# Kernel optimization log

Measured on AMD Instinct MI355X. Metric: run time of the kernel, lower is better.

The kernel has to match this reference:

```python
import jax, jax.numpy as jnp
import numpy as np

V, N, K, D = 2, 100000, 8, 128
TAU = 1.0
LOG_2PI = float(np.log(2.0 * np.pi))


def setup_inputs() -> dict:
    key = jax.random.key(0)
    k1, k2, k3 = jax.random.split(key, 3)
    z = jax.random.normal(k1, (V, N, D), dtype=jnp.float32)
    phi = jnp.ones((V, K), dtype=jnp.float32) / K
    mu = jax.random.normal(k2, (V, K, D), dtype=jnp.float32)
    # sigma: identity (as in torch init) plus a small symmetric PSD perturbation
    a = 0.05 * jax.random.normal(k3, (V, K, D, D), dtype=jnp.float32)
    sigma = jnp.eye(D, dtype=jnp.float32) + jnp.einsum('vkde,vkfe->vkdf', a, a)
    return {"z": z, "phi": phi, "mu": mu, "sigma": sigma}


def _compute_energy(z, phi, mu, sigma):
    # z: [N, D]; phi: [K]; mu: [K, D]; sigma: [K, D, D]
    eps_eye = 1e-6 * jnp.eye(D, dtype=z.dtype)
    sigma_stable = sigma + eps_eye  # [K, D, D]
    inv_sigma = jnp.linalg.inv(sigma_stable)
    det_sigma = jnp.clip(jnp.linalg.det(sigma_stable), 1e-6, None)  # [K]
    diff = z[:, None, :] - mu[None, :, :]  # [N, K, D]
    maha = jnp.einsum('nkd,kde,nke->nk', diff, inv_sigma, diff)  # [N, K]
    log_pi = jax.nn.log_softmax(phi)  # [K]
    log_prob = (-0.5 * maha
                - 0.5 * D * LOG_2PI
                - 0.5 * jnp.log(det_sigma)[None, :]
                + log_pi[None, :])  # [N, K]
    energy = -jax.nn.logsumexp(log_prob, axis=1)  # [N]
    penalty = jnp.sum(1.0 / (jnp.diagonal(sigma_stable, axis1=-2, axis2=-1) + 1e-12))
    return energy, penalty


def reference(z, phi, mu, sigma):
    # vmap over views; energies_v: [V, N]
    energies_v, penalties = jax.vmap(_compute_energy)(z, phi, mu, sigma)
    energies = energies_v.T  # [N, V]
    total_energies = jnp.sum(energies)
    total_penalty = jnp.sum(penalties)
    weights = jax.nn.softmax(-energies / TAU, axis=1)  # [N, V]
    return energies, weights, total_energies, total_penalty
```

## Files before the change

### kernel.cpp

```cpp
#include <hip/hip_runtime.h>
#include <math.h>

#define V 2
#define NN 100000
#define KK 8
#define DD 128
#define TILE_N 128
#define SL 132
#define NT 782
#define CH 8
#define CPX 13
#define NPAD 100096
#define LOG2PI 1.8378770664093454f
#define LOG_1EM6 -13.815510557964274f

#define IMG_PB 40960
#define IMG_LO_US 10240

#define LF_B   1114112
#define LF_STRIDE 69632
#define BV_B   2228224
#define C_B    2236416
#define MAHA_B 2236480

#define OUT_W_OFF (NN*V)
#define OUT_TE (2*NN*V)
#define OUT_TP (2*NN*V + 1)

typedef __attribute__((ext_vector_type(8))) short bf16x8;
typedef __attribute__((ext_vector_type(4))) float f32x4;
typedef __attribute__((ext_vector_type(4))) unsigned u32x4;

__device__ __forceinline__ unsigned short f2bf_rtn(float f) {
    unsigned u = __builtin_bit_cast(unsigned, f);
    unsigned r = u + 0x7FFFu + ((u >> 16) & 1u);
    return (unsigned short)(r >> 16);
}
__device__ __forceinline__ float bf2f(unsigned short h) {
    unsigned u = ((unsigned)h) << 16;
    return __builtin_bit_cast(float, u);
}

__device__ __forceinline__ void cvt_pair(float f0, float f1, unsigned& hi, unsigned& lo) {
    unsigned u0 = __builtin_bit_cast(unsigned, f0);
    unsigned u1 = __builtin_bit_cast(unsigned, f1);
    hi = __builtin_amdgcn_perm(u1, u0, 0x07060302u);
    float r0 = f0 - __builtin_bit_cast(float, u0 & 0xFFFF0000u);
    float r1 = f1 - __builtin_bit_cast(float, u1 & 0xFFFF0000u);
    unsigned v0 = __builtin_bit_cast(unsigned, r0) + 0x8000u;
    unsigned v1 = __builtin_bit_cast(unsigned, r1) + 0x8000u;
    lo = __builtin_amdgcn_perm(v1, v0, 0x07060302u);
}

__global__ void zero_kernel(float* out) {
    int t = threadIdx.x;
    if (t < 2) out[OUT_TE + t] = 0.0f;
}

__global__ __launch_bounds__(256) void prep_chol(const float* __restrict__ phi,
                                                 const float* __restrict__ mu,
                                                 const float* __restrict__ sigma,
                                                 void* __restrict__ wsv,
                                                 float* __restrict__ out) {
    __shared__ float Lf[DD * SL];
    __shared__ float P[8][SL];
    __shared__ float dvec[DD];
    __shared__ float mulds[DD];
    __shared__ float red[256];
    __shared__ float Bv[8];
    __shared__ float Bb[DD];

    const int tid = threadIdx.x;
    const int vk  = blockIdx.x;
    const int v   = vk >> 3;
    const int k   = vk & 7;
    const int R   = tid >> 4;
    const int C   = tid & 15;

    if (tid < DD) mulds[tid] = mu[vk * DD + tid];

    float A[8][8];
    const float* sig = sigma + (size_t)vk * DD * DD;
    float pen = 0.0f;
    #pragma unroll
    for (int a = 0; a < 8; ++a) {
        const float4* p4 = (const float4*)(sig + (size_t)(8 * R + a) * DD + 8 * C);
        float4 x = p4[0], y = p4[1];
        A[a][0] = x.x; A[a][1] = x.y; A[a][2] = x.z; A[a][3] = x.w;
        A[a][4] = y.x; A[a][5] = y.y; A[a][6] = y.z; A[a][7] = y.w;
        if (R == C) A[a][a] += 1e-6f;
    }
    if (R == C) {
        #pragma unroll
        for (int a = 0; a < 8; ++a) pen += 1.0f / (A[a][a] + 1e-12f);
    }

    for (int i = tid; i < DD * SL; i += 256) Lf[i] = 0.0f;

    red[tid] = pen;
    __syncthreads();
    for (int s = 128; s > 0; s >>= 1) {
        if (tid < s) red[tid] += red[tid + s];
        __syncthreads();
    }
    if (tid == 0) atomicAdd(&out[OUT_TP], red[0]);
    __syncthreads();

    for (int p = 0; p < 16; ++p) {
        if (C == p && R >= p) {
            #pragma unroll
            for (int b = 0; b < 8; ++b) {
                *(float4*)&P[b][8 * R]     = make_float4(A[0][b], A[1][b], A[2][b], A[3][b]);
                *(float4*)&P[b][8 * R + 4] = make_float4(A[4][b], A[5][b], A[6][b], A[7][b]);
            }
        }
        __syncthreads();

        if (tid < 64) {
            const int lane = tid;
            const int r1 = 8 * p + lane;
            const int r2 = r1 + 64;
            const bool ok2 = (r2 < DD);
            float pr1[8], pr2[8], rs[8];
            #pragma unroll
            for (int j = 0; j < 8; ++j) {
                pr1[j] = (r1 < DD) ? P[j][r1] : 0.0f;
                pr2[j] = ok2 ? P[j][r2] : 0.0f;
            }
            #pragma unroll
            for (int j = 0; j < 8; ++j) {
                if (lane >= j && lane < 8) Bv[lane] = pr1[j];
                __builtin_amdgcn_wave_barrier();
                float bv[8];
                #pragma unroll
                for (int m = 0; m < 8; ++m) bv[m] = Bv[m];
                __builtin_amdgcn_wave_barrier();
                float piv = bv[j];
                if (lane == j) dvec[8 * p + j] = piv;
                float inv2 = 1.0f / piv;
                rs[j] = rsqrtf(piv);
                float m1 = pr1[j] * inv2;
                float m2 = pr2[j] * inv2;
                #pragma unroll
                for (int j2 = 0; j2 < 8; ++j2) {
                    if (j2 > j) {
                        if (lane > j) pr1[j2] -= m1 * bv[j2];
                        pr2[j2] -= m2 * bv[j2];
                    }
                }
            }
            #pragma unroll
            for (int j = 0; j < 8; ++j) {
                if (r1 < DD) {
                    float v1 = (lane >= j) ? pr1[j] * rs[j] : 0.0f;
                    P[j][r1] = v1;
                    Lf[r1 * SL + 8 * p + j] = v1;
                }
                if (ok2) {
                    float v2 = pr2[j] * rs[j];
                    P[j][r2] = v2;
                    Lf[r2 * SL + 8 * p + j] = v2;
                }
            }
        }
        __syncthreads();

        if (C > p && R >= p) {
            #pragma unroll
            for (int j = 0; j < 8; ++j) {
                float4 a0 = *(const float4*)&P[j][8 * R];
                float4 a1 = *(const float4*)&P[j][8 * R + 4];
                float4 b0 = *(const float4*)&P[j][8 * C];
                float4 b1 = *(const float4*)&P[j][8 * C + 4];
                float ra[8] = {a0.x, a0.y, a0.z, a0.w, a1.x, a1.y, a1.z, a1.w};
                float rb[8] = {b0.x, b0.y, b0.z, b0.w, b1.x, b1.y, b1.z, b1.w};
                #pragma unroll
                for (int a = 0; a < 8; ++a)
                    #pragma unroll
                    for (int b = 0; b < 8; ++b)
                        A[a][b] -= ra[a] * rb[b];
            }
        }
        __syncthreads();
    }

    if (tid < 64) {
        const int lane = tid;
        float acc0 = mulds[lane];
        float acc1 = mulds[lane + 64];
        for (int j = 0; j < DD; ++j) {
            if (j < 64) { if (lane == j)      Bb[j] = acc0 / Lf[j * SL + j]; }
            else        { if (lane == j - 64) Bb[j] = acc1 / Lf[j * SL + j]; }
            __builtin_amdgcn_wave_barrier();
            float bj = Bb[j];
            __builtin_amdgcn_wave_barrier();
            if (lane > j)      acc0 -= Lf[lane * SL + j] * bj;
            if (lane + 64 > j) acc1 -= Lf[(lane + 64) * SL + j] * bj;
        }
    }
    __syncthreads();
    if (tid < DD) ((float*)((char*)wsv + BV_B))[vk * DD + tid] = Bb[tid];

    {
        float4* Lg = (float4*)((char*)wsv + LF_B + (size_t)vk * LF_STRIDE);
        const float4* Ls4 = (const float4*)Lf;
        for (int i = tid; i < DD * SL / 4; i += 256) Lg[i] = Ls4[i];
    }

    red[tid] = (tid < DD) ? logf(dvec[tid]) : 0.0f;
    __syncthreads();
    for (int s = 128; s > 0; s >>= 1) {
        if (tid < s) red[tid] += red[tid + s];
        __syncthreads();
    }
    if (tid == 0) {
        float logdet_c = fmaxf(red[0], LOG_1EM6);
        const float* ph = phi + v * KK;
        float m = ph[0];
        for (int i = 1; i < KK; ++i) m = fmaxf(m, ph[i]);
        float s = 0.0f;
        for (int i = 0; i < KK; ++i) s += expf(ph[i] - m);
        float logpi = ph[k] - m - logf(s);
        ((float*)((char*)wsv + C_B))[vk] = logpi - 0.5f * logdet_c - 0.5f * (float)DD * LOG2PI;
    }
}

__global__ __launch_bounds__(256) void prep_trsm(void* __restrict__ wsv) {
    __shared__ float Ls[DD * SL];
    __shared__ float Wc[32][SL];

    const int tid = threadIdx.x;
    const int vk  = blockIdx.x >> 2;
    const int cg  = blockIdx.x & 3;

    const float4* Lg = (const float4*)((const char*)wsv + LF_B + (size_t)vk * LF_STRIDE);
    float4* Ls4 = (float4*)Ls;
    for (int i = tid; i < DD * SL / 4; i += 256) Ls4[i] = Lg[i];
    __syncthreads();

    const int c   = tid >> 3;
    const int par = tid & 7;
    const int j   = 4 * c + cg;

    for (int e = par; e < SL; e += 8) Wc[c][e] = 0.0f;
    if (par == 0) Wc[c][j] = 1.0f / Ls[j * SL + j];
    __builtin_amdgcn_wave_barrier();

    const int pbase = j & ~3;
    for (int i = j + 1; i < DD; ++i) {
        float s = 0.0f;
        for (int p4 = pbase + 4 * par; p4 < i; p4 += 32) {
            float4 lf = *(const float4*)&Ls[i * SL + p4];
            float4 wc = *(const float4*)&Wc[c][p4];
            s += lf.x * wc.x + lf.y * wc.y + lf.z * wc.z + lf.w * wc.w;
        }
        s += __shfl_xor(s, 1, 64);
        s += __shfl_xor(s, 2, 64);
        s += __shfl_xor(s, 4, 64);
        if (par == 0) Wc[c][i] = -s / Ls[i * SL + i];
        __builtin_amdgcn_wave_barrier();
    }

    unsigned short* Gh = (unsigned short*)((char*)wsv + (size_t)vk * IMG_PB);
    for (int i2 = par; i2 < DD; i2 += 8) {
        const int b = i2 >> 5;
        if ((j >> 5) > b) continue;
        const int ri   = i2 & 31;
        const int hbb  = (b == 0 ? 0 : b == 1 ? 2048 : b == 2 ? 6144 : 12288);
        const int cb   = ri * 64 * (b + 1) + (j >> 3) * 16;
        const int sw   = cb ^ ((ri & 7) << 4);
        const int us   = ((hbb + sw) >> 1) + (j & 7);
        float f = (i2 >= j) ? Wc[c][i2] : 0.0f;
        unsigned short h = f2bf_rtn(f);
        unsigned short l = f2bf_rtn(f - bf2f(h));
        Gh[us] = h;
        Gh[us + IMG_LO_US] = l;
    }
}

__global__ __launch_bounds__(256) void maha_kernel(const float* __restrict__ z,
                                                   void* __restrict__ wsv) {
    __shared__ unsigned short wl[IMG_PB / 2];

    const int tid  = threadIdx.x;
    const int lane = tid & 63;
    const int wave = tid >> 6;
    const int quad = lane >> 4;
    const int l16  = lane & 15;
    const int swz  = (l16 & 7) << 4;

    const int bi    = blockIdx.x;
    const int xcd   = bi & 7;
    const int jj    = bi >> 3;
    const int r     = jj & 15;
    const int lc    = jj >> 4;
    const int chunk = xcd * CPX + lc;
    const int vv    = r >> 3;

    if (chunk * CH >= NT) return;

    {
        const char* src = (const char*)wsv + (size_t)r * IMG_PB;
        char* dst = (char*)wl;
        const int lane_off = wave * 1024 + lane * 16;
        #pragma unroll
        for (int t = 0; t < 10; ++t)
            __builtin_amdgcn_global_load_lds(
                (const __attribute__((address_space(1))) void*)(src + t * 4096 + lane_off),
                (__attribute__((address_space(3))) void*)(dst + t * 4096 + wave * 1024),
                16, 0, 0);
    }

    float blr[8];
    {
        const float* bvp = (const float*)((const char*)wsv + BV_B) + r * DD;
        #pragma unroll
        for (int nt = 0; nt < 8; ++nt) blr[nt] = bvp[nt * 16 + l16];
    }
    __syncthreads();

    const float* zbase = z + (size_t)vv * NN * DD;
    float* mrow = (float*)((char*)wsv + MAHA_B) + (size_t)r * NPAD;
    const char* wlb = (const char*)wl;

    for (int ti = 0; ti < CH; ++ti) {
        const int t = chunk * CH + ti;
        if (t >= NT) break;
        const int n0 = t * TILE_N;

        float4 raw[2][4][2];
        #pragma unroll
        for (int mt = 0; mt < 2; ++mt) {
            const int n = n0 + wave * 32 + mt * 16 + l16;
            const bool ok = (n < NN);
            const float* zp = zbase + (size_t)n * DD + quad * 8;
            #pragma unroll
            for (int ds = 0; ds < 4; ++ds) {
                if (ok) {
                    raw[mt][ds][0] = *(const float4*)(zp + ds * 32);
                    raw[mt][ds][1] = *(const float4*)(zp + ds * 32 + 4);
                } else {
                    raw[mt][ds][0] = make_float4(0.f, 0.f, 0.f, 0.f);
                    raw[mt][ds][1] = make_float4(0.f, 0.f, 0.f, 0.f);
                }
            }
        }

        u32x4 zh[2][4], zl[2][4];
        #pragma unroll
        for (int mt = 0; mt < 2; ++mt)
            #pragma unroll
            for (int ds = 0; ds < 4; ++ds) {
                float4 a = raw[mt][ds][0];
                float4 b = raw[mt][ds][1];
                unsigned h0, l0, h1, l1, h2, l2, h3, l3;
                cvt_pair(a.x, a.y, h0, l0);
                cvt_pair(a.z, a.w, h1, l1);
                cvt_pair(b.x, b.y, h2, l2);
                cvt_pair(b.z, b.w, h3, l3);
                u32x4 th, tl;
                th[0] = h0; th[1] = h1; th[2] = h2; th[3] = h3;
                tl[0] = l0; tl[1] = l1; tl[2] = l2; tl[3] = l3;
                zh[mt][ds] = th;
                zl[mt][ds] = tl;
            }

        float p[2][4] = {{0.f, 0.f, 0.f, 0.f}, {0.f, 0.f, 0.f, 0.f}};
        #pragma unroll
        for (int nt = 0; nt < 8; ++nt) {
            const int b   = nt >> 1;
            const int ri  = ((nt & 1) << 4) + l16;
            const int hbb = (b == 0 ? 0 : b == 1 ? 2048 : b == 2 ? 6144 : 12288);
            f32x4 a0 = (f32x4)(-blr[nt]);
            f32x4 a1 = (f32x4)(-blr[nt]);
            #pragma unroll
            for (int ds = 0; ds <= (nt >> 1); ++ds) {
                const int g   = ds * 4 + quad;
                const int off = hbb + ((ri * 64 * (b + 1) + g * 16) ^ swz);
                bf16x8 bh  = *(const bf16x8*)(wlb + off);
                bf16x8 blo = *(const bf16x8*)(wlb + off + 2 * IMG_LO_US);
                bf16x8 ah0 = __builtin_bit_cast(bf16x8, zh[0][ds]);
                bf16x8 al0 = __builtin_bit_cast(bf16x8, zl[0][ds]);
                bf16x8 ah1 = __builtin_bit_cast(bf16x8, zh[1][ds]);
                bf16x8 al1 = __builtin_bit_cast(bf16x8, zl[1][ds]);
                a0 = __builtin_amdgcn_mfma_f32_16x16x32_bf16(ah0, bh,  a0, 0, 0, 0);
                a0 = __builtin_amdgcn_mfma_f32_16x16x32_bf16(ah0, blo, a0, 0, 0, 0);
                a0 = __builtin_amdgcn_mfma_f32_16x16x32_bf16(al0, bh,  a0, 0, 0, 0);
                a1 = __builtin_amdgcn_mfma_f32_16x16x32_bf16(ah1, bh,  a1, 0, 0, 0);
                a1 = __builtin_amdgcn_mfma_f32_16x16x32_bf16(ah1, blo, a1, 0, 0, 0);
                a1 = __builtin_amdgcn_mfma_f32_16x16x32_bf16(al1, bh,  a1, 0, 0, 0);
            }
            #pragma unroll
            for (int reg = 0; reg < 4; ++reg) {
                p[0][reg] += a0[reg] * a0[reg];
                p[1][reg] += a1[reg] * a1[reg];
            }
        }

        #pragma unroll
        for (int mt = 0; mt < 2; ++mt) {
            float sv[4];
            #pragma unroll
            for (int reg = 0; reg < 4; ++reg) {
                float s = p[mt][reg];
                s += __shfl_xor(s, 1, 64);
                s += __shfl_xor(s, 2, 64);
                s += __shfl_xor(s, 4, 64);
                s += __shfl_xor(s, 8, 64);
                sv[reg] = s;
            }
            if (l16 == 0)
                *(float4*)&mrow[n0 + wave * 32 + mt * 16 + quad * 4] =
                    make_float4(sv[0], sv[1], sv[2], sv[3]);
        }
    }
}

__global__ __launch_bounds__(256) void finalize_kernel(const void* __restrict__ wsv,
                                                       float* __restrict__ out) {
    __shared__ float red[256];
    __shared__ float clds[16];

    const int tid = threadIdx.x;
    if (tid < 16) clds[tid] = ((const float*)((const char*)wsv + C_B))[tid];
    __syncthreads();

    const float* mahap = (const float*)((const char*)wsv + MAHA_B);
    const int n = blockIdx.x * 256 + tid;
    float esum = 0.0f;

    if (n < NN) {
        float ev[V];
        #pragma unroll
        for (int vv = 0; vv < V; ++vv) {
            float lp[KK];
            float m = -1e30f;
            #pragma unroll
            for (int k = 0; k < KK; ++k) {
                int r = vv * KK + k;
                lp[k] = -0.5f * mahap[(size_t)r * NPAD + n] + clds[r];
                m = fmaxf(m, lp[k]);
            }
            float s = 0.0f;
            #pragma unroll
            for (int k = 0; k < KK; ++k) s += expf(lp[k] - m);
            ev[vv] = -(m + logf(s));
        }
        float e0 = ev[0], e1 = ev[1];
        float m = fmaxf(-e0, -e1);
        float x0 = expf(-e0 - m);
        float x1 = expf(-e1 - m);
        float inv = 1.0f / (x0 + x1);
        out[(size_t)n * V + 0] = e0;
        out[(size_t)n * V + 1] = e1;
        out[OUT_W_OFF + (size_t)n * V + 0] = x0 * inv;
        out[OUT_W_OFF + (size_t)n * V + 1] = x1 * inv;
        esum = e0 + e1;
    }

    red[tid] = esum;
    __syncthreads();
    for (int s = 128; s > 0; s >>= 1) {
        if (tid < s) red[tid] += red[tid + s];
        __syncthreads();
    }
    if (tid == 0) atomicAdd(&out[OUT_TE], red[0]);
}

extern "C" void kernel_launch(void* const* d_in, const int* in_sizes, int n_in,
                              void* d_out, int out_size, void* d_ws, size_t ws_size,
                              hipStream_t stream) {
    const float* z     = (const float*)d_in[0];
    const float* phi   = (const float*)d_in[1];
    const float* mu    = (const float*)d_in[2];
    const float* sigma = (const float*)d_in[3];
    float* out = (float*)d_out;

    hipLaunchKernelGGL(zero_kernel, dim3(1), dim3(64), 0, stream, out);
    hipLaunchKernelGGL(prep_chol, dim3(V * KK), dim3(256), 0, stream, phi, mu, sigma, d_ws, out);
    hipLaunchKernelGGL(prep_trsm, dim3(64), dim3(256), 0, stream, d_ws);
    hipLaunchKernelGGL(maha_kernel, dim3(8 * CPX * 16), dim3(256), 0, stream, z, d_ws);
    hipLaunchKernelGGL(finalize_kernel, dim3((NPAD + 255) / 256), dim3(256), 0, stream, d_ws, out);
}
```

Baseline: 393.3 us.

## Switch Mahalanobis MFMA to 32x32x16 with transposed operands and in-register reduction

Replaces the 16x16x32 bf16 MFMA tiling with 32x32x16 MFMAs where the Cholesky-like factor is the A operand and z rows are B. Each lane now owns one sample column, so the squared-norm reduction is mostly in-register with a single cross-half shuffle instead of four xor shuffles per output. The bias vector moves into shared memory and is read as float4. This aims to cut shuffle and accumulator overhead and use the larger MFMA shape, but it changes the register footprint (16-wide accumulator) and the z load pattern.

```diff
diff --git a/kernel.cpp b/kernel.cpp
--- a/kernel.cpp
+++ b/kernel.cpp
@@ -27,9 +27,10 @@
 #define OUT_TE (2*NN*V)
 #define OUT_TP (2*NN*V + 1)
 
-typedef __attribute__((ext_vector_type(8))) short bf16x8;
-typedef __attribute__((ext_vector_type(4))) float f32x4;
-typedef __attribute__((ext_vector_type(4))) unsigned u32x4;
+typedef __attribute__((ext_vector_type(8)))  short bf16x8;
+typedef __attribute__((ext_vector_type(4)))  float f32x4;
+typedef __attribute__((ext_vector_type(16))) float f32x16;
+typedef __attribute__((ext_vector_type(4)))  unsigned u32x4;
 
 __device__ __forceinline__ unsigned short f2bf_rtn(float f) {
     unsigned u = __builtin_bit_cast(unsigned, f);
@@ -281,13 +282,14 @@
 __global__ __launch_bounds__(256) void maha_kernel(const float* __restrict__ z,
                                                    void* __restrict__ wsv) {
     __shared__ unsigned short wl[IMG_PB / 2];
+    __shared__ float bl_s[DD];
 
     const int tid  = threadIdx.x;
     const int lane = tid & 63;
     const int wave = tid >> 6;
-    const int quad = lane >> 4;
-    const int l16  = lane & 15;
-    const int swz  = (l16 & 7) << 4;
+    const int rl   = lane & 31;
+    const int h    = lane >> 5;
+    const int swz  = (lane & 7) << 4;
 
     const int bi    = blockIdx.x;
     const int xcd   = bi & 7;
@@ -310,13 +312,7 @@
                 (__attribute__((address_space(3))) void*)(dst + t * 4096 + wave * 1024),
                 16, 0, 0);
     }
-
-    float blr[8];
-    {
-        const float* bvp = (const float*)((const char*)wsv + BV_B) + r * DD;
-        #pragma unroll
-        for (int nt = 0; nt < 8; ++nt) blr[nt] = bvp[nt * 16 + l16];
-    }
+    if (tid < DD) bl_s[tid] = ((const float*)((const char*)wsv + BV_B))[r * DD + tid];
     __syncthreads();
 
     const float* zbase = z + (size_t)vv * NN * DD;
@@ -328,91 +324,70 @@
         if (t >= NT) break;
         const int n0 = t * TILE_N;
 
-        float4 raw[2][4][2];
-        #pragma unroll
-        for (int mt = 0; mt < 2; ++mt) {
-            const int n = n0 + wave * 32 + mt * 16 + l16;
-            const bool ok = (n < NN);
-            const float* zp = zbase + (size_t)n * DD + quad * 8;
-            #pragma unroll
-            for (int ds = 0; ds < 4; ++ds) {
-                if (ok) {
-                    raw[mt][ds][0] = *(const float4*)(zp + ds * 32);
-                    raw[mt][ds][1] = *(const float4*)(zp + ds * 32 + 4);
-                } else {
-                    raw[mt][ds][0] = make_float4(0.f, 0.f, 0.f, 0.f);
-                    raw[mt][ds][1] = make_float4(0.f, 0.f, 0.f, 0.f);
-                }
-            }
-        }
-
-        u32x4 zh[2][4], zl[2][4];
-        #pragma unroll
-        for (int mt = 0; mt < 2; ++mt)
-            #pragma unroll
-            for (int ds = 0; ds < 4; ++ds) {
-                float4 a = raw[mt][ds][0];
-                float4 b = raw[mt][ds][1];
-                unsigned h0, l0, h1, l1, h2, l2, h3, l3;
-                cvt_pair(a.x, a.y, h0, l0);
-                cvt_pair(a.z, a.w, h1, l1);
-                cvt_pair(b.x, b.y, h2, l2);
-                cvt_pair(b.z, b.w, h3, l3);
-                u32x4 th, tl;
-                th[0] = h0; th[1] = h1; th[2] = h2; th[3] = h3;
-                tl[0] = l0; tl[1] = l1; tl[2] = l2; tl[3] = l3;
-                zh[mt][ds] = th;
-                zl[mt][ds] = tl;
-            }
-
-        float p[2][4] = {{0.f, 0.f, 0.f, 0.f}, {0.f, 0.f, 0.f, 0.f}};
-        #pragma unroll
-        for (int nt = 0; nt < 8; ++nt) {
-            const int b   = nt >> 1;
-            const int ri  = ((nt & 1) << 4) + l16;
-            const int hbb = (b == 0 ? 0 : b == 1 ? 2048 : b == 2 ? 6144 : 12288);
-            f32x4 a0 = (f32x4)(-blr[nt]);
-            f32x4 a1 = (f32x4)(-blr[nt]);
-            #pragma unroll
-            for (int ds = 0; ds <= (nt >> 1); ++ds) {
-                const int g   = ds * 4 + quad;
-                const int off = hbb + ((ri * 64 * (b + 1) + g * 16) ^ swz);
-                bf16x8 bh  = *(const bf16x8*)(wlb + off);
-                bf16x8 blo = *(const bf16x8*)(wlb + off + 2 * IMG_LO_US);
-                bf16x8 ah0 = __builtin_bit_cast(bf16x8, zh[0][ds]);
-                bf16x8 al0 = __builtin_bit_cast(bf16x8, zl[0][ds]);
-                bf16x8 ah1 = __builtin_bit_cast(bf16x8, zh[1][ds]);
-                bf16x8 al1 = __builtin_bit_cast(bf16x8, zl[1][ds]);
-                a0 = __builtin_amdgcn_mfma_f32_16x16x32_bf16(ah0, bh,  a0, 0, 0, 0);
-                a0 = __builtin_amdgcn_mfma_f32_16x16x32_bf16(ah0, blo, a0, 0, 0, 0);
-                a0 = __builtin_amdgcn_mfma_f32_16x16x32_bf16(al0, bh,  a0, 0, 0, 0);
-                a1 = __builtin_amdgcn_mfma_f32_16x16x32_bf16(ah1, bh,  a1, 0, 0, 0);
-                a1 = __builtin_amdgcn_mfma_f32_16x16x32_bf16(ah1, blo, a1, 0, 0, 0);
-                a1 = __builtin_amdgcn_mfma_f32_16x16x32_bf16(al1, bh,  a1, 0, 0, 0);
-            }
-            #pragma unroll
-            for (int reg = 0; reg < 4; ++reg) {
-                p[0][reg] += a0[reg] * a0[reg];
-                p[1][reg] += a1[reg] * a1[reg];
-            }
-        }
-
-        #pragma unroll
-        for (int mt = 0; mt < 2; ++mt) {
-            float sv[4];
-            #pragma unroll
-            for (int reg = 0; reg < 4; ++reg) {
-                float s = p[mt][reg];
-                s += __shfl_xor(s, 1, 64);
-                s += __shfl_xor(s, 2, 64);
-                s += __shfl_xor(s, 4, 64);
-                s += __shfl_xor(s, 8, 64);
-                sv[reg] = s;
-            }
-            if (l16 == 0)
-                *(float4*)&mrow[n0 + wave * 32 + mt * 16 + quad * 4] =
-                    make_float4(sv[0], sv[1], sv[2], sv[3]);
-        }
+        const int n   = n0 + wave * 32 + rl;
+        const bool ok = (n < NN);
+        const float* zp = zbase + (size_t)n * DD + h * 8;
+
+        float4 raw[8][2];
+        #pragma unroll
+        for (int s = 0; s < 8; ++s) {
+            if (ok) {
+                raw[s][0] = *(const float4*)(zp + s * 16);
+                raw[s][1] = *(const float4*)(zp + s * 16 + 4);
+            } else {
+                raw[s][0] = make_float4(0.f, 0.f, 0.f, 0.f);
+                raw[s][1] = make_float4(0.f, 0.f, 0.f, 0.f);
+            }
+        }
+
+        u32x4 zh8[8], zl8[8];
+        #pragma unroll
+        for (int s = 0; s < 8; ++s) {
+            float4 a = raw[s][0];
+            float4 b = raw[s][1];
+            unsigned h0, l0, h1, l1, h2, l2, h3, l3;
+            cvt_pair(a.x, a.y, h0, l0);
+            cvt_pair(a.z, a.w, h1, l1);
+            cvt_pair(b.x, b.y, h2, l2);
+            cvt_pair(b.z, b.w, h3, l3);
+            u32x4 th, tl;
+            th[0] = h0; th[1] = h1; th[2] = h2; th[3] = h3;
+            tl[0] = l0; tl[1] = l1; tl[2] = l2; tl[3] = l3;
+            zh8[s] = th;
+            zl8[s] = tl;
+        }
+
+        float pa = 0.0f;
+        #pragma unroll
+        for (int R = 0; R < 4; ++R) {
+            const int hb = (R == 0 ? 0 : R == 1 ? 2048 : R == 2 ? 6144 : 12288);
+            const int st = 64 * (R + 1);
+            f32x16 D = (f32x16)(0.0f);
+            #pragma unroll
+            for (int s = 0; s <= 2 * R + 1; ++s) {
+                const int g   = 2 * s + h;
+                const int off = hb + ((rl * st + g * 16) ^ swz);
+                bf16x8 wh  = *(const bf16x8*)(wlb + off);
+                bf16x8 wlo = *(const bf16x8*)(wlb + off + 2 * IMG_LO_US);
+                bf16x8 zh = __builtin_bit_cast(bf16x8, zh8[s]);
+                bf16x8 zl = __builtin_bit_cast(bf16x8, zl8[s]);
+                D = __builtin_amdgcn_mfma_f32_32x32x16_bf16(wh,  zh, D, 0, 0, 0);
+                D = __builtin_amdgcn_mfma_f32_32x32x16_bf16(wlo, zh, D, 0, 0, 0);
+                D = __builtin_amdgcn_mfma_f32_32x32x16_bf16(wh,  zl, D, 0, 0, 0);
+            }
+            #pragma unroll
+            for (int q = 0; q < 4; ++q) {
+                float4 bq = *(const float4*)&bl_s[32 * R + 8 * q + 4 * h];
+                float t0 = D[4 * q + 0] - bq.x;
+                float t1 = D[4 * q + 1] - bq.y;
+                float t2 = D[4 * q + 2] - bq.z;
+                float t3 = D[4 * q + 3] - bq.w;
+                pa += t0 * t0 + t1 * t1 + t2 * t2 + t3 * t3;
+            }
+        }
+
+        pa += __shfl_xor(pa, 32, 64);
+        if (lane < 32) mrow[n0 + wave * 32 + rl] = pa;
     }
 }
 
```

Measured after the change: 383.7 us. 1.02x faster.
